# Kernel tuning notes

Measured on AMD Instinct MI355X. Metric: run time of the kernel, lower is better.

## Reference

```python
import jax, jax.numpy as jnp
import numpy as np

VOCAB, EMB, H, OUT = 32000, 512, 1024, 32000
SEQ, B = 512, 64

def setup_inputs() -> dict:
    key = jax.random.key(0)
    ks = jax.random.split(key, 16)
    sc = lambda *s: 1.0 / np.sqrt(s[-1])
    return {
        "x": jax.random.randint(ks[0], (B,), 0, VOCAB),
        "encoder_states": jax.random.normal(ks[1], (SEQ, B, 2 * H), jnp.float32),
        "hidden": jax.random.normal(ks[2], (1, B, H), jnp.float32),
        "cell": jax.random.normal(ks[3], (1, B, H), jnp.float32),
        "emb_table": jax.random.normal(ks[4], (VOCAB, EMB), jnp.float32),
        "energy_W": jax.random.normal(ks[5], (1, 3 * H), jnp.float32) * sc(1, 3 * H),
        "energy_b": jnp.zeros((1,), jnp.float32),
        "W_ih": jax.random.normal(ks[6], (4 * H, 2 * H + EMB), jnp.float32) * sc(1, H),
        "W_hh": jax.random.normal(ks[7], (4 * H, H), jnp.float32) * sc(1, H),
        "b_ih": jnp.zeros((4 * H,), jnp.float32),
        "b_hh": jnp.zeros((4 * H,), jnp.float32),
        "fc_W": jax.random.normal(ks[8], (OUT, H), jnp.float32) * sc(1, H),
        "fc_b": jnp.zeros((OUT,), jnp.float32),
    }

def reference(x, encoder_states, hidden, cell, emb_table, energy_W, energy_b,
              W_ih, W_hh, b_ih, b_hh, fc_W, fc_b):
    S = encoder_states.shape[0]
    emb = emb_table[x]                                     # [B, E] (dropout is identity at p=0)
    h_rep = jnp.broadcast_to(hidden, (S,) + hidden.shape[1:])   # [S, B, H]
    cat = jnp.concatenate([h_rep, encoder_states], axis=2)      # [S, B, 3H]
    energy = jax.nn.relu(jnp.einsum('sbk,ok->sbo', cat, energy_W) + energy_b)  # [S, B, 1]
    attn = jax.nn.softmax(energy[..., 0], axis=0)                # softmax over seq dim -> [S, B]
    context = jnp.einsum('sb,sbd->bd', attn, encoder_states)     # [B, 2H]
    rnn_in = jnp.concatenate([context, emb], axis=1)             # [B, 2H+E]
    gates = rnn_in @ W_ih.T + b_ih + hidden[0] @ W_hh.T + b_hh   # [B, 4H]
    i, f, g, o = jnp.split(gates, 4, axis=1)
    i, f, o = jax.nn.sigmoid(i), jax.nn.sigmoid(f), jax.nn.sigmoid(o)
    g = jnp.tanh(g)
    c_new = f * cell[0] + i * g
    h_new = o * jnp.tanh(c_new)
    preds = h_new @ fc_W.T + fc_b                                # [B, OUT]
    return preds, h_new[None], c_new[None]
```

## Files before the change

### kernel.cpp

```cpp
#include <hip/hip_runtime.h>

#define S_LEN 512
#define BATCH 64
#define HDIM  1024
#define TWOH  2048
#define EMB   512
#define KDIM  2560
#define KTOT  3584
#define VOUT  32000

#define WS_MS    64
#define WS_CTX   2112
#define WS_GP    WS_CTX
#define WS_RNNB  (WS_CTX + 64*16*2048)
#define WS_HB16  (WS_RNNB + 114688)

typedef __attribute__((ext_vector_type(8))) short bf16x8;
typedef __attribute__((ext_vector_type(4))) float f32x4;

__device__ __forceinline__ float sigmoidf_(float x) { return 1.f/(1.f+__expf(-x)); }

__device__ __forceinline__ unsigned short f2bf(float f) {
  union { float f; unsigned u; } v; v.f = f;
  return (unsigned short)((v.u + 0x7fffu + ((v.u >> 16) & 1u)) >> 16);
}

__device__ __forceinline__ bf16x8 cvt_frag(const float4& a, const float4& b) {
  bf16x8 r;
  r[0] = (short)f2bf(a.x); r[1] = (short)f2bf(a.y);
  r[2] = (short)f2bf(a.z); r[3] = (short)f2bf(a.w);
  r[4] = (short)f2bf(b.x); r[5] = (short)f2bf(b.y);
  r[6] = (short)f2bf(b.z); r[7] = (short)f2bf(b.w);
  return r;
}

__global__ __launch_bounds__(256) void k_attn(const float* __restrict__ enc,
                                              const float* __restrict__ eW,
                                              const float* __restrict__ eb,
                                              const float* __restrict__ hidden,
                                              float* __restrict__ ws_ms,
                                              float* __restrict__ ws_ctx) {
  __shared__ float lds_ms[4][2];
  __shared__ float lds_ctx[4][2048];
  const int lane  = threadIdx.x & 63;
  const int wave  = threadIdx.x >> 6;
  const int chunk = blockIdx.x;
  const int b     = blockIdx.y;

  float hba = 0.f;
  for (int k = lane; k < HDIM; k += 64) hba += hidden[b*HDIM + k] * eW[k];
#pragma unroll
  for (int st = 32; st >= 1; st >>= 1) hba += __shfl_xor(hba, st, 64);
  const float hb = hba + eb[0];

  float4 w4[8];
#pragma unroll
  for (int k = 0; k < 8; ++k)
    w4[k] = *reinterpret_cast<const float4*>(eW + HDIM + 4*lane + 256*k);

  const int s0 = chunk*32 + wave*8;
  const float* base = enc + ((size_t)(s0*BATCH + b))*TWOH + 4*lane;

  float m = 0.f, ssum = 0.f;
  float4 ctx[8];
#pragma unroll
  for (int k = 0; k < 8; ++k) ctx[k] = make_float4(0.f, 0.f, 0.f, 0.f);

  float4 va[8], vb[8];
#pragma unroll
  for (int k = 0; k < 8; ++k) va[k] = *reinterpret_cast<const float4*>(base + 256*k);

#define ATTN_STEP(VCUR, VNXT, I)                                              \
  {                                                                           \
    if ((I) < 7) {                                                            \
      const float* pn = base + (size_t)((I)+1)*BATCH*TWOH;                    \
      _Pragma("unroll")                                                       \
      for (int k = 0; k < 8; ++k)                                             \
        VNXT[k] = *reinterpret_cast<const float4*>(pn + 256*k);               \
    }                                                                         \
    float a = 0.f;                                                            \
    _Pragma("unroll")                                                         \
    for (int k = 0; k < 8; ++k)                                               \
      a += VCUR[k].x*w4[k].x + VCUR[k].y*w4[k].y +                            \
           VCUR[k].z*w4[k].z + VCUR[k].w*w4[k].w;                             \
    _Pragma("unroll")                                                         \
    for (int st = 1; st < 64; st <<= 1) a += __shfl_xor(a, st, 64);           \
    const float e = fmaxf(a + hb, 0.f);                                       \
    if (e > m) {                                                              \
      const float sc = __expf(m - e);                                         \
      ssum = ssum*sc + 1.f;                                                   \
      _Pragma("unroll")                                                       \
      for (int k = 0; k < 8; ++k) {                                           \
        ctx[k].x = fmaf(ctx[k].x, sc, VCUR[k].x);                             \
        ctx[k].y = fmaf(ctx[k].y, sc, VCUR[k].y);                             \
        ctx[k].z = fmaf(ctx[k].z, sc, VCUR[k].z);                             \
        ctx[k].w = fmaf(ctx[k].w, sc, VCUR[k].w);                             \
      }                                                                       \
      m = e;                                                                  \
    } else {                                                                  \
      const float pw = __expf(e - m);                                         \
      ssum += pw;                                                             \
      _Pragma("unroll")                                                       \
      for (int k = 0; k < 8; ++k) {                                           \
        ctx[k].x = fmaf(pw, VCUR[k].x, ctx[k].x);                             \
        ctx[k].y = fmaf(pw, VCUR[k].y, ctx[k].y);                             \
        ctx[k].z = fmaf(pw, VCUR[k].z, ctx[k].z);                             \
        ctx[k].w = fmaf(pw, VCUR[k].w, ctx[k].w);                             \
      }                                                                       \
    }                                                                         \
  }

  ATTN_STEP(va, vb, 0)
  ATTN_STEP(vb, va, 1)
  ATTN_STEP(va, vb, 2)
  ATTN_STEP(vb, va, 3)
  ATTN_STEP(va, vb, 4)
  ATTN_STEP(vb, va, 5)
  ATTN_STEP(va, vb, 6)
  ATTN_STEP(vb, va, 7)
#undef ATTN_STEP

  if (lane == 0) { lds_ms[wave][0] = m; lds_ms[wave][1] = ssum; }
  __syncthreads();
  const float M = fmaxf(fmaxf(lds_ms[0][0], lds_ms[1][0]),
                        fmaxf(lds_ms[2][0], lds_ms[3][0]));
  const float wsc = __expf(m - M);
  float ssum_c = 0.f;
#pragma unroll
  for (int w = 0; w < 4; ++w) ssum_c += __expf(lds_ms[w][0] - M) * lds_ms[w][1];
#pragma unroll
  for (int k = 0; k < 8; ++k) {
    float4 c = ctx[k];
    c.x *= wsc; c.y *= wsc; c.z *= wsc; c.w *= wsc;
    *reinterpret_cast<float4*>(&lds_ctx[wave][4*lane + 256*k]) = c;
  }
  __syncthreads();
  float* outp = ws_ctx + ((size_t)b*16 + chunk)*TWOH;
  for (int d = threadIdx.x; d < TWOH; d += 256)
    outp[d] = lds_ctx[0][d] + lds_ctx[1][d] + lds_ctx[2][d] + lds_ctx[3][d];
  if (threadIdx.x == 0) {
    ws_ms[((size_t)b*16 + chunk)*2]     = M;
    ws_ms[((size_t)b*16 + chunk)*2 + 1] = ssum_c;
  }
}

__global__ __launch_bounds__(256) void k_combine(const float* __restrict__ ws_ms,
                                                 const float* __restrict__ ws_ctx,
                                                 const float* __restrict__ hidden,
                                                 const float* __restrict__ emb_table,
                                                 const int* __restrict__ x,
                                                 unsigned short* __restrict__ rnnB) {
  const int b = blockIdx.x;
  float mc[16], sc[16];
#pragma unroll
  for (int c = 0; c < 16; ++c) {
    mc[c] = ws_ms[(b*16 + c)*2];
    sc[c] = ws_ms[(b*16 + c)*2 + 1];
  }
  float M = mc[0];
#pragma unroll
  for (int c = 1; c < 16; ++c) M = fmaxf(M, mc[c]);
  float wc[16], Ssum = 0.f;
#pragma unroll
  for (int c = 0; c < 16; ++c) { wc[c] = __expf(mc[c] - M); Ssum += wc[c]*sc[c]; }
  const float inv = 1.f / Ssum;
  unsigned short* rb = rnnB + (size_t)b*KTOT;
  for (int d = threadIdx.x; d < TWOH; d += 256) {
    float a = 0.f;
#pragma unroll
    for (int c = 0; c < 16; ++c) a += wc[c] * ws_ctx[((size_t)b*16 + c)*TWOH + d];
    rb[d] = f2bf(a * inv);
  }
  const int xb = x[b];
  for (int e = threadIdx.x; e < EMB; e += 256)
    rb[TWOH + e] = f2bf(emb_table[(size_t)xb*EMB + e]);
  for (int k = threadIdx.x; k < HDIM; k += 256)
    rb[KDIM + k] = f2bf(hidden[b*HDIM + k]);
}

__global__ __launch_bounds__(256) void k_gates(const unsigned short* __restrict__ rnnB,
                                               const float* __restrict__ W_ih,
                                               const float* __restrict__ W_hh,
                                               float* __restrict__ ws_gp) {
  const int lane = threadIdx.x & 63;
  const int wave = threadIdx.x >> 6;
  const int part = blockIdx.x & 7;
  const int rg   = blockIdx.x >> 3;
  const int row0 = rg*64 + wave*16;
  const int mlo  = lane & 15;
  const int kg   = lane >> 4;
  const int j    = row0 + mlo;

  f32x4 acc0 = {0.f,0.f,0.f,0.f}, acc1 = acc0, acc2 = acc0, acc3 = acc0;

  for (int k0 = 0; k0 < 448; k0 += 64) {
    const int kb0 = part*448 + k0;
    const int kb1 = kb0 + 32;
    const float* ws0 = (kb0 < KDIM) ? (W_ih + (size_t)j*KDIM + kb0 + kg*8)
                                    : (W_hh + (size_t)j*HDIM + (kb0 - KDIM) + kg*8);
    const float* ws1 = (kb1 < KDIM) ? (W_ih + (size_t)j*KDIM + kb1 + kg*8)
                                    : (W_hh + (size_t)j*HDIM + (kb1 - KDIM) + kg*8);
    const float4 wa0 = *reinterpret_cast<const float4*>(ws0);
    const float4 wb0 = *reinterpret_cast<const float4*>(ws0 + 4);
    const float4 wa1 = *reinterpret_cast<const float4*>(ws1);
    const float4 wb1 = *reinterpret_cast<const float4*>(ws1 + 4);

    const size_t ko0 = (size_t)kb0 + kg*8;
    const size_t ko1 = (size_t)kb1 + kg*8;
    const unsigned short* rp0 = rnnB + (size_t)mlo*KTOT;
    const bf16x8 b00 = *reinterpret_cast<const bf16x8*>(rp0 + ko0);
    const bf16x8 b10 = *reinterpret_cast<const bf16x8*>(rp0 + 16*KTOT + ko0);
    const bf16x8 b20 = *reinterpret_cast<const bf16x8*>(rp0 + 32*KTOT + ko0);
    const bf16x8 b30 = *reinterpret_cast<const bf16x8*>(rp0 + 48*KTOT + ko0);
    const bf16x8 b01 = *reinterpret_cast<const bf16x8*>(rp0 + ko1);
    const bf16x8 b11 = *reinterpret_cast<const bf16x8*>(rp0 + 16*KTOT + ko1);
    const bf16x8 b21 = *reinterpret_cast<const bf16x8*>(rp0 + 32*KTOT + ko1);
    const bf16x8 b31 = *reinterpret_cast<const bf16x8*>(rp0 + 48*KTOT + ko1);

    const bf16x8 af0 = cvt_frag(wa0, wb0);
    const bf16x8 af1 = cvt_frag(wa1, wb1);

    acc0 = __builtin_amdgcn_mfma_f32_16x16x32_bf16(af0, b00, acc0, 0, 0, 0);
    acc1 = __builtin_amdgcn_mfma_f32_16x16x32_bf16(af0, b10, acc1, 0, 0, 0);
    acc2 = __builtin_amdgcn_mfma_f32_16x16x32_bf16(af0, b20, acc2, 0, 0, 0);
    acc3 = __builtin_amdgcn_mfma_f32_16x16x32_bf16(af0, b30, acc3, 0, 0, 0);
    acc0 = __builtin_amdgcn_mfma_f32_16x16x32_bf16(af1, b01, acc0, 0, 0, 0);
    acc1 = __builtin_amdgcn_mfma_f32_16x16x32_bf16(af1, b11, acc1, 0, 0, 0);
    acc2 = __builtin_amdgcn_mfma_f32_16x16x32_bf16(af1, b21, acc2, 0, 0, 0);
    acc3 = __builtin_amdgcn_mfma_f32_16x16x32_bf16(af1, b31, acc3, 0, 0, 0);
  }

  const int mbase = row0 + kg*4;
#define G_ST(ACC, N)                                                          \
  {                                                                           \
    _Pragma("unroll")                                                         \
    for (int jj = 0; jj < 4; ++jj)                                            \
      ws_gp[((size_t)part*4096 + mbase + jj)*64 + ((N)*16 + mlo)] = ACC[jj];  \
  }
  G_ST(acc0, 0) G_ST(acc1, 1) G_ST(acc2, 2) G_ST(acc3, 3)
#undef G_ST
}

__global__ __launch_bounds__(256) void k_lstm(const float* __restrict__ ws_gp,
                                              const float* __restrict__ b_ih,
                                              const float* __restrict__ b_hh,
                                              const float* __restrict__ cell,
                                              float* __restrict__ out_h,
                                              float* __restrict__ out_c,
                                              unsigned short* __restrict__ hB) {
  const int id = blockIdx.x*256 + threadIdx.x;
  const int h = id >> 6, b = id & 63;
  float g[4];
#pragma unroll
  for (int gg = 0; gg < 4; ++gg) {
    const int j = gg*1024 + h;
    float v = b_ih[j] + b_hh[j];
#pragma unroll
    for (int p = 0; p < 8; ++p) v += ws_gp[((size_t)p*4096 + j)*64 + b];
    g[gg] = v;
  }
  const float iv = sigmoidf_(g[0]);
  const float fv = sigmoidf_(g[1]);
  const float gv = tanhf(g[2]);
  const float ov = sigmoidf_(g[3]);
  const float cold = cell[b*HDIM + h];
  const float cn = fmaf(fv, cold, iv*gv);
  const float hn = ov * tanhf(cn);
  out_h[b*HDIM + h] = hn;
  out_c[b*HDIM + h] = cn;
  hB[(size_t)b*HDIM + h] = f2bf(hn);
}

__global__ __launch_bounds__(256) void k_fc(const unsigned short* __restrict__ hB,
                                            const float* __restrict__ fc_W,
                                            const float* __restrict__ fc_b,
                                            float* __restrict__ preds) {
  const int lane = threadIdx.x & 63;
  const int wave = threadIdx.x >> 6;
  const int row0 = (blockIdx.x*4 + wave)*16;
  const int mlo  = lane & 15;
  const int kg   = lane >> 4;

  const float* wrow = fc_W + (size_t)(row0 + mlo)*HDIM + kg*8;
  const unsigned short* hp = hB + (size_t)mlo*HDIM + kg*8;

  f32x4 acc0 = {0.f,0.f,0.f,0.f}, acc1 = acc0, acc2 = acc0, acc3 = acc0;

  for (int k0 = 0; k0 < HDIM; k0 += 64) {
    const float4 wa0 = *reinterpret_cast<const float4*>(wrow + k0);
    const float4 wb0 = *reinterpret_cast<const float4*>(wrow + k0 + 4);
    const float4 wa1 = *reinterpret_cast<const float4*>(wrow + k0 + 32);
    const float4 wb1 = *reinterpret_cast<const float4*>(wrow + k0 + 36);

    const bf16x8 b00 = *reinterpret_cast<const bf16x8*>(hp + k0);
    const bf16x8 b10 = *reinterpret_cast<const bf16x8*>(hp + 16*HDIM + k0);
    const bf16x8 b20 = *reinterpret_cast<const bf16x8*>(hp + 32*HDIM + k0);
    const bf16x8 b30 = *reinterpret_cast<const bf16x8*>(hp + 48*HDIM + k0);
    const bf16x8 b01 = *reinterpret_cast<const bf16x8*>(hp + k0 + 32);
    const bf16x8 b11 = *reinterpret_cast<const bf16x8*>(hp + 16*HDIM + k0 + 32);
    const bf16x8 b21 = *reinterpret_cast<const bf16x8*>(hp + 32*HDIM + k0 + 32);
    const bf16x8 b31 = *reinterpret_cast<const bf16x8*>(hp + 48*HDIM + k0 + 32);

    const bf16x8 af0 = cvt_frag(wa0, wb0);
    const bf16x8 af1 = cvt_frag(wa1, wb1);

    acc0 = __builtin_amdgcn_mfma_f32_16x16x32_bf16(af0, b00, acc0, 0, 0, 0);
    acc1 = __builtin_amdgcn_mfma_f32_16x16x32_bf16(af0, b10, acc1, 0, 0, 0);
    acc2 = __builtin_amdgcn_mfma_f32_16x16x32_bf16(af0, b20, acc2, 0, 0, 0);
    acc3 = __builtin_amdgcn_mfma_f32_16x16x32_bf16(af0, b30, acc3, 0, 0, 0);
    acc0 = __builtin_amdgcn_mfma_f32_16x16x32_bf16(af1, b01, acc0, 0, 0, 0);
    acc1 = __builtin_amdgcn_mfma_f32_16x16x32_bf16(af1, b11, acc1, 0, 0, 0);
    acc2 = __builtin_amdgcn_mfma_f32_16x16x32_bf16(af1, b21, acc2, 0, 0, 0);
    acc3 = __builtin_amdgcn_mfma_f32_16x16x32_bf16(af1, b31, acc3, 0, 0, 0);
  }

  const int mbase = row0 + kg*4;
  const float4 bias = make_float4(fc_b[mbase], fc_b[mbase+1],
                                  fc_b[mbase+2], fc_b[mbase+3]);
#define FC_STORE(ACC, N)                                                      \
  {                                                                           \
    float4 st = make_float4(ACC[0] + bias.x, ACC[1] + bias.y,                 \
                            ACC[2] + bias.z, ACC[3] + bias.w);                \
    *reinterpret_cast<float4*>(preds + (size_t)((N)*16 + mlo)*VOUT + mbase) = st; \
  }
  FC_STORE(acc0, 0) FC_STORE(acc1, 1) FC_STORE(acc2, 2) FC_STORE(acc3, 3)
#undef FC_STORE
}

extern "C" void kernel_launch(void* const* d_in, const int* in_sizes, int n_in,
                              void* d_out, int out_size, void* d_ws, size_t ws_size,
                              hipStream_t stream) {
  const int*   x      = (const int*)  d_in[0];
  const float* enc    = (const float*)d_in[1];
  const float* hidden = (const float*)d_in[2];
  const float* cell   = (const float*)d_in[3];
  const float* embt   = (const float*)d_in[4];
  const float* eW     = (const float*)d_in[5];
  const float* eb     = (const float*)d_in[6];
  const float* W_ih   = (const float*)d_in[7];
  const float* W_hh   = (const float*)d_in[8];
  const float* b_ih   = (const float*)d_in[9];
  const float* b_hh   = (const float*)d_in[10];
  const float* fc_W   = (const float*)d_in[11];
  const float* fc_b   = (const float*)d_in[12];

  float* out   = (float*)d_out;
  float* preds = out;
  float* out_h = out + (size_t)BATCH*VOUT;
  float* out_c = out_h + BATCH*HDIM;
  float* ws    = (float*)d_ws;
  unsigned short* rnnB = (unsigned short*)(ws + WS_RNNB);
  unsigned short* hB   = (unsigned short*)(ws + WS_HB16);

  k_attn<<<dim3(16, 64), 256, 0, stream>>>(enc, eW, eb, hidden, ws + WS_MS, ws + WS_CTX);
  k_combine<<<64, 256, 0, stream>>>(ws + WS_MS, ws + WS_CTX, hidden, embt, x, rnnB);
  k_gates<<<512, 256, 0, stream>>>(rnnB, W_ih, W_hh, ws + WS_GP);
  k_lstm<<<256, 256, 0, stream>>>(ws + WS_GP, b_ih, b_hh, cell, out_h, out_c, hB);
  k_fc<<<500, 256, 0, stream>>>(hB, fc_W, fc_b, preds);
}
```

Before: 149.2 us.

## Split FC GEMM along K with reduction kernel and widen combine grid

The output projection is split into two K halves across twice as many blocks. Half the partial sums go into a workspace buffer and a new reduction kernel adds them together with the bias. The combine kernel is also spread over a 2D grid so each thread handles one element instead of 64 blocks looping. This raises parallelism on a 256-CU GPU where 500 blocks underfill the device. The cost is an extra kernel launch plus writing and re-reading roughly 16 MB of partial results.

```diff
diff --git a/kernel.cpp b/kernel.cpp
--- a/kernel.cpp
+++ b/kernel.cpp
@@ -12,6 +12,7 @@
 #define WS_MS    64
 #define WS_CTX   2112
 #define WS_GP    WS_CTX
+#define WS_FP    WS_CTX
 #define WS_RNNB  (WS_CTX + 64*16*2048)
 #define WS_HB16  (WS_RNNB + 114688)
 
@@ -150,32 +151,34 @@
                                                  const float* __restrict__ emb_table,
                                                  const int* __restrict__ x,
                                                  unsigned short* __restrict__ rnnB) {
-  const int b = blockIdx.x;
-  float mc[16], sc[16];
-#pragma unroll
-  for (int c = 0; c < 16; ++c) {
-    mc[c] = ws_ms[(b*16 + c)*2];
-    sc[c] = ws_ms[(b*16 + c)*2 + 1];
-  }
-  float M = mc[0];
-#pragma unroll
-  for (int c = 1; c < 16; ++c) M = fmaxf(M, mc[c]);
-  float wc[16], Ssum = 0.f;
-#pragma unroll
-  for (int c = 0; c < 16; ++c) { wc[c] = __expf(mc[c] - M); Ssum += wc[c]*sc[c]; }
-  const float inv = 1.f / Ssum;
+  const int b = blockIdx.y;
+  const int k = blockIdx.x*256 + threadIdx.x;
   unsigned short* rb = rnnB + (size_t)b*KTOT;
-  for (int d = threadIdx.x; d < TWOH; d += 256) {
+
+  if (k < TWOH) {
+    float mc[16], sc[16];
+#pragma unroll
+    for (int c = 0; c < 16; ++c) {
+      mc[c] = ws_ms[(b*16 + c)*2];
+      sc[c] = ws_ms[(b*16 + c)*2 + 1];
+    }
+    float M = mc[0];
+#pragma unroll
+    for (int c = 1; c < 16; ++c) M = fmaxf(M, mc[c]);
+    float wc[16], Ssum = 0.f;
+#pragma unroll
+    for (int c = 0; c < 16; ++c) { wc[c] = __expf(mc[c] - M); Ssum += wc[c]*sc[c]; }
+    const float inv = 1.f / Ssum;
     float a = 0.f;
 #pragma unroll
-    for (int c = 0; c < 16; ++c) a += wc[c] * ws_ctx[((size_t)b*16 + c)*TWOH + d];
-    rb[d] = f2bf(a * inv);
-  }
-  const int xb = x[b];
-  for (int e = threadIdx.x; e < EMB; e += 256)
-    rb[TWOH + e] = f2bf(emb_table[(size_t)xb*EMB + e]);
-  for (int k = threadIdx.x; k < HDIM; k += 256)
-    rb[KDIM + k] = f2bf(hidden[b*HDIM + k]);
+    for (int c = 0; c < 16; ++c) a += wc[c] * ws_ctx[((size_t)b*16 + c)*TWOH + k];
+    rb[k] = f2bf(a * inv);
+  } else if (k < KDIM) {
+    const int xb = x[b];
+    rb[k] = f2bf(emb_table[(size_t)xb*EMB + (k - TWOH)]);
+  } else {
+    rb[k] = f2bf(hidden[b*HDIM + (k - KDIM)]);
+  }
 }
 
 __global__ __launch_bounds__(256) void k_gates(const unsigned short* __restrict__ rnnB,
@@ -273,20 +276,22 @@
 
 __global__ __launch_bounds__(256) void k_fc(const unsigned short* __restrict__ hB,
                                             const float* __restrict__ fc_W,
-                                            const float* __restrict__ fc_b,
-                                            float* __restrict__ preds) {
+                                            float* __restrict__ preds,
+                                            float* __restrict__ fpart) {
   const int lane = threadIdx.x & 63;
   const int wave = threadIdx.x >> 6;
-  const int row0 = (blockIdx.x*4 + wave)*16;
+  const int rb   = blockIdx.x >> 1;
+  const int part = blockIdx.x & 1;
+  const int row0 = (rb*4 + wave)*16;
   const int mlo  = lane & 15;
   const int kg   = lane >> 4;
 
-  const float* wrow = fc_W + (size_t)(row0 + mlo)*HDIM + kg*8;
-  const unsigned short* hp = hB + (size_t)mlo*HDIM + kg*8;
+  const float* wrow = fc_W + (size_t)(row0 + mlo)*HDIM + part*512 + kg*8;
+  const unsigned short* hp = hB + (size_t)mlo*HDIM + part*512 + kg*8;
 
   f32x4 acc0 = {0.f,0.f,0.f,0.f}, acc1 = acc0, acc2 = acc0, acc3 = acc0;
 
-  for (int k0 = 0; k0 < HDIM; k0 += 64) {
+  for (int k0 = 0; k0 < 512; k0 += 64) {
     const float4 wa0 = *reinterpret_cast<const float4*>(wrow + k0);
     const float4 wb0 = *reinterpret_cast<const float4*>(wrow + k0 + 4);
     const float4 wa1 = *reinterpret_cast<const float4*>(wrow + k0 + 32);
@@ -314,17 +319,29 @@
     acc3 = __builtin_amdgcn_mfma_f32_16x16x32_bf16(af1, b31, acc3, 0, 0, 0);
   }
 
+  float* dst = part ? fpart : preds;
   const int mbase = row0 + kg*4;
-  const float4 bias = make_float4(fc_b[mbase], fc_b[mbase+1],
-                                  fc_b[mbase+2], fc_b[mbase+3]);
 #define FC_STORE(ACC, N)                                                      \
   {                                                                           \
-    float4 st = make_float4(ACC[0] + bias.x, ACC[1] + bias.y,                 \
-                            ACC[2] + bias.z, ACC[3] + bias.w);                \
-    *reinterpret_cast<float4*>(preds + (size_t)((N)*16 + mlo)*VOUT + mbase) = st; \
+    float4 st = make_float4(ACC[0], ACC[1], ACC[2], ACC[3]);                  \
+    *reinterpret_cast<float4*>(dst + (size_t)((N)*16 + mlo)*VOUT + mbase) = st; \
   }
   FC_STORE(acc0, 0) FC_STORE(acc1, 1) FC_STORE(acc2, 2) FC_STORE(acc3, 3)
 #undef FC_STORE
+}
+
+__global__ __launch_bounds__(256) void k_fcred(float* __restrict__ preds,
+                                               const float* __restrict__ fpart,
+                                               const float* __restrict__ fc_b) {
+  const size_t i4 = (size_t)blockIdx.x*256 + threadIdx.x;
+  const size_t idx = i4*4;
+  const int r = (int)(idx % VOUT);
+  const float4 p0 = *reinterpret_cast<const float4*>(preds + idx);
+  const float4 p1 = *reinterpret_cast<const float4*>(fpart + idx);
+  const float4 bb = *reinterpret_cast<const float4*>(fc_b + r);
+  float4 st = make_float4(p0.x + p1.x + bb.x, p0.y + p1.y + bb.y,
+                          p0.z + p1.z + bb.z, p0.w + p1.w + bb.w);
+  *reinterpret_cast<float4*>(preds + idx) = st;
 }
 
 extern "C" void kernel_launch(void* const* d_in, const int* in_sizes, int n_in,
@@ -353,8 +370,9 @@
   unsigned short* hB   = (unsigned short*)(ws + WS_HB16);
 
   k_attn<<<dim3(16, 64), 256, 0, stream>>>(enc, eW, eb, hidden, ws + WS_MS, ws + WS_CTX);
-  k_combine<<<64, 256, 0, stream>>>(ws + WS_MS, ws + WS_CTX, hidden, embt, x, rnnB);
+  k_combine<<<dim3(14, 64), 256, 0, stream>>>(ws + WS_MS, ws + WS_CTX, hidden, embt, x, rnnB);
   k_gates<<<512, 256, 0, stream>>>(rnnB, W_ih, W_hh, ws + WS_GP);
   k_lstm<<<256, 256, 0, stream>>>(ws + WS_GP, b_ih, b_hh, cell, out_h, out_c, hB);
-  k_fc<<<500, 256, 0, stream>>>(hB, fc_W, fc_b, preds);
-}
+  k_fc<<<1000, 256, 0, stream>>>(hB, fc_W, preds, ws + WS_FP);
+  k_fcred<<<2000, 256, 0, stream>>>(preds, ws + WS_FP, fc_b);
+}
```

Result: no change. 150.9 us (+1.2%).
